# Performance work log

Hardware: AMD Instinct MI355X
Metric: run time of the kernel (lower is better)

Reference implementation:

```python
import jax, jax.numpy as jnp
import numpy as np

N = 200000      # nodes
E = 1600000     # directed edges (before self-loops)
G = 5000        # graphs (molecules)
IN, HID, OUT, HEADS = 128, 128, 128, 3


def gat_layer(x, src, dst, W, a_src, a_dst, b, heads, out_dim, concat):
    n = x.shape[0]
    h = (x @ W).reshape(n, heads, out_dim)                 # [N,H,F]
    al_s = jnp.einsum('nhf,hf->nh', h, a_src)              # [N,H]
    al_d = jnp.einsum('nhf,hf->nh', h, a_dst)
    e = jax.nn.leaky_relu(al_s[src] + al_d[dst], 0.2)      # [E,H]
    m = jax.ops.segment_max(e, dst, num_segments=n)        # softmax over incoming edges
    ex = jnp.exp(e - m[dst])
    den = jax.ops.segment_sum(ex, dst, num_segments=n)
    alpha = ex / (den[dst] + 1e-16)                        # [E,H]
    msg = h[src] * alpha[..., None]                        # [E,H,F]
    agg = jax.ops.segment_sum(msg, dst, num_segments=n)    # [N,H,F]
    agg = agg.reshape(n, heads * out_dim) if concat else agg.mean(axis=1)
    return agg + b


def setup_inputs() -> dict:
    key = jax.random.key(0)
    ks = jax.random.split(key, 16)
    d = {}
    d['x'] = jax.random.normal(ks[0], (N, IN), dtype=jnp.float32)
    d['edge_index'] = jax.random.randint(ks[1], (2, E), 0, N, dtype=jnp.int64)
    d['batch'] = jnp.sort(jax.random.randint(ks[2], (N,), 0, G, dtype=jnp.int64))
    s = 0.1
    d['W1'] = jax.random.normal(ks[3], (IN, HEADS * HID), jnp.float32) * s
    d['a1s'] = jax.random.normal(ks[4], (HEADS, HID), jnp.float32) * s
    d['a1d'] = jax.random.normal(ks[5], (HEADS, HID), jnp.float32) * s
    d['b1'] = jnp.zeros((HEADS * HID,), jnp.float32)
    d['W2'] = jax.random.normal(ks[6], (HEADS * HID, HEADS * HID), jnp.float32) * s
    d['a2s'] = jax.random.normal(ks[7], (HEADS, HID), jnp.float32) * s
    d['a2d'] = jax.random.normal(ks[8], (HEADS, HID), jnp.float32) * s
    d['b2'] = jnp.zeros((HEADS * HID,), jnp.float32)
    d['W3'] = jax.random.normal(ks[9], (HEADS * HID, OUT), jnp.float32) * s
    d['a3s'] = jax.random.normal(ks[10], (1, OUT), jnp.float32) * s
    d['a3d'] = jax.random.normal(ks[11], (1, OUT), jnp.float32) * s
    d['b3'] = jnp.zeros((OUT,), jnp.float32)
    return d


def reference(x, edge_index, batch, W1, a1s, a1d, b1, W2, a2s, a2d, b2, W3, a3s, a3d, b3):
    # PyG GATConv default add_self_loops=True
    loops = jnp.arange(N, dtype=edge_index.dtype)
    src = jnp.concatenate([edge_index[0], loops])
    dst = jnp.concatenate([edge_index[1], loops])
    h = jax.nn.leaky_relu(gat_layer(x, src, dst, W1, a1s, a1d, b1, HEADS, HID, True), 0.2)
    h = jax.nn.leaky_relu(gat_layer(h, src, dst, W2, a2s, a2d, b2, HEADS, HID, True), 0.2)
    h = jax.nn.leaky_relu(gat_layer(h, src, dst, W3, a3s, a3d, b3, 1, OUT, False), 0.2)
    # global mean pool over graphs
    sums = jax.ops.segment_sum(h, batch, num_segments=G)            # [G,OUT]
    cnt = jax.ops.segment_sum(jnp.ones((N,), h.dtype), batch, num_segments=G)
    return sums / jnp.maximum(cnt, 1.0)[:, None]
```

## Files before the change

### kernel.cpp

```cpp
#include <hip/hip_runtime.h>
#include <hip/hip_bf16.h>
#include <math.h>

#define LRELU_SLOPE 0.2f
typedef __hip_bfloat16 bf16;
typedef __hip_bfloat162 bf16x2;

typedef short s8v __attribute__((ext_vector_type(8)));
typedef float f4v __attribute__((ext_vector_type(4)));

__device__ __forceinline__ float lrelu(float v) { return v > 0.f ? v : LRELU_SLOPE * v; }
__device__ __forceinline__ float b2f(short b) {
  return __uint_as_float(((unsigned)(unsigned short)b) << 16);
}

__device__ __forceinline__ void st2(bf16* p, float x, float y) {
  float2 f{x, y};
  *(bf16x2*)p = __float22bfloat162_rn(f);
}
__device__ __forceinline__ void st2(float* p, float x, float y) {
  *(float2*)p = float2{x, y};
}

__device__ __forceinline__ void st2_nt(bf16* p, float x, float y) {
  float2 f{x, y};
  bf16x2 v = __float22bfloat162_rn(f);
  __builtin_nontemporal_store(*(unsigned int*)&v, (unsigned int*)p);
}
__device__ __forceinline__ void st2_nt(float* p, float x, float y) {
  __builtin_nontemporal_store(x, p);
  __builtin_nontemporal_store(y, p + 1);
}


__global__ void k_zero(unsigned int* __restrict__ p, long n) {
  long i = (long)blockIdx.x * blockDim.x + threadIdx.x;
  if (i < n) p[i] = 0u;
}

__global__ void k_zero_out(float* __restrict__ out, int n) {
  int i = blockIdx.x * blockDim.x + threadIdx.x;
  if (i < n) out[i] = 0.f;
}


__global__ void k_cvt(const float* __restrict__ x, bf16* __restrict__ xb, long n) {
  long i = (long)blockIdx.x * blockDim.x + threadIdx.x;
  if (i < n) xb[i] = __float2bfloat16(x[i]);
}

__global__ void k_tw(const float* __restrict__ W, bf16* __restrict__ Wt, int K, int NN) {
  int i = blockIdx.x * blockDim.x + threadIdx.x;
  if (i >= K * NN) return;
  int k = i / NN, n = i - k * NN;
  Wt[(size_t)n * K + k] = __float2bfloat16(W[i]);
}


__global__ void k_hist(const int* __restrict__ dst, int* __restrict__ deg, int E, int Et) {
  int e = blockIdx.x * blockDim.x + threadIdx.x;
  if (e >= Et) return;
  int d = (e < E) ? dst[e] : (e - E);
  atomicAdd(&deg[d], 1);
}

__global__ void k_hist1(const int* __restrict__ idx, int* __restrict__ deg, int n) {
  int i = blockIdx.x * blockDim.x + threadIdx.x;
  if (i < n) atomicAdd(&deg[idx[i]], 1);
}

__global__ void k_scan1(const int* __restrict__ deg, int* __restrict__ offs,
                        int* __restrict__ bsum, int n) {
  __shared__ int sd[256];
  int t = threadIdx.x;
  int base = blockIdx.x * 1024 + t * 4;
  int v[4]; int tsum = 0;
#pragma unroll
  for (int i = 0; i < 4; ++i) { v[i] = (base + i < n) ? deg[base + i] : 0; tsum += v[i]; }
  sd[t] = tsum;
  __syncthreads();
  for (int off = 1; off < 256; off <<= 1) {
    int x = (t >= off) ? sd[t - off] : 0;
    __syncthreads();
    sd[t] += x;
    __syncthreads();
  }
  int excl = sd[t] - tsum;
#pragma unroll
  for (int i = 0; i < 4; ++i) { if (base + i < n) offs[base + i] = excl; excl += v[i]; }
  if (t == 255) bsum[blockIdx.x] = sd[255];
}

__global__ void k_scan2(int* bsum, int nb) {
  if (threadIdx.x == 0 && blockIdx.x == 0) {
    int run = 0;
    for (int i = 0; i < nb; ++i) { int t = bsum[i]; bsum[i] = run; run += t; }
  }
}

__global__ void k_scan3(int* __restrict__ offs, const int* __restrict__ bsum, int n, int total) {
  int t = threadIdx.x;
  int base = blockIdx.x * 1024 + t * 4;
  int add = bsum[blockIdx.x];
#pragma unroll
  for (int i = 0; i < 4; ++i) if (base + i < n) offs[base + i] += add;
  if (blockIdx.x == 0 && t == 0) offs[n] = total;
}

__global__ void k_scatter(const int* __restrict__ src, const int* __restrict__ dst,
                          const int* __restrict__ offs, int* __restrict__ cur,
                          int* __restrict__ ssrc, int E, int Et) {
  int e = blockIdx.x * blockDim.x + threadIdx.x;
  if (e >= Et) return;
  int s, d;
  if (e < E) { s = src[e]; d = dst[e]; } else { s = d = e - E; }
  int pos = offs[d] + atomicAdd(&cur[d], 1);
  ssrc[pos] = s;
}


__global__ __launch_bounds__(256) void k_gemm_mfma(const bf16* __restrict__ A,
                                                   const bf16* __restrict__ Wt,
                                                   bf16* __restrict__ C,
                                                   int K, int NN) {
  __shared__ __align__(16) short sA[64 * 64];
  int t = threadIdx.x;
  int wv = t >> 6, lane = t & 63;
  int quad = lane >> 4, l15 = lane & 15;
  size_t bm0 = (size_t)blockIdx.x * 64;
  int bn0 = blockIdx.y * 64;
  const bf16* Ab = A + bm0 * K;
  const bf16* Bp = Wt + (size_t)(bn0 + wv * 16 + l15) * K;
  f4v acc[4] = {f4v{0,0,0,0}, f4v{0,0,0,0}, f4v{0,0,0,0}, f4v{0,0,0,0}};

  for (int kb = 0; kb < K; kb += 64) {
#pragma unroll
    for (int j = 0; j < 2; ++j) {
      int idx = j * 256 + t;
      int row = idx >> 3, p = idx & 7;
      int c = p ^ (row & 7);
      const bf16* g = Ab + (size_t)row * K + kb + c * 8;
      __builtin_amdgcn_global_load_lds(
          (const __attribute__((address_space(1))) void*)g,
          (__attribute__((address_space(3))) void*)((char*)sA + (size_t)(j * 256 + wv * 64) * 16),
          16, 0, 0);
    }
    __syncthreads();
#pragma unroll
    for (int kk = 0; kk < 2; ++kk) {
      s8v bfrag = *(const s8v*)(Bp + kb + kk * 32 + quad * 8);
#pragma unroll
      for (int ms = 0; ms < 4; ++ms) {
        int row = ms * 16 + l15;
        int pos = (kk * 4 + quad) ^ (row & 7);
        s8v afrag = *(const s8v*)((const char*)sA + (size_t)row * 128 + pos * 16);
        acc[ms] = __builtin_amdgcn_mfma_f32_16x16x32_bf16(afrag, bfrag, acc[ms], 0, 0, 0);
      }
    }
    __syncthreads();
  }
  int coln = bn0 + wv * 16 + l15;
#pragma unroll
  for (int ms = 0; ms < 4; ++ms)
#pragma unroll
    for (int r = 0; r < 4; ++r)
      C[(bm0 + ms * 16 + quad * 4 + r) * NN + coln] = __float2bfloat16(acc[ms][r]);
}


template <int H>
__global__ void k_al(const bf16* __restrict__ h, const float* __restrict__ as,
                     const float* __restrict__ ad, float* __restrict__ al_s,
                     float* __restrict__ al_d, int N) {
  int n = (blockIdx.x * blockDim.x + threadIdx.x) >> 6;
  int lane = threadIdx.x & 63;
  if (n >= N) return;
  int hd = lane >> 4;
  bool active = (hd < H);
  int hdc = active ? hd : 0;
  int f8 = (lane & 15) * 8;
  const bf16* hp = h + (size_t)n * (H * 128) + hdc * 128 + f8;
  s8v hv = *(const s8v*)hp;
  float ss = 0.f, sd = 0.f;
#pragma unroll
  for (int i = 0; i < 8; ++i) {
    float v = b2f(hv[i]);
    ss += v * as[hdc * 128 + f8 + i];
    sd += v * ad[hdc * 128 + f8 + i];
  }
#pragma unroll
  for (int off = 8; off; off >>= 1) {
    ss += __shfl_xor(ss, off, 64);
    sd += __shfl_xor(sd, off, 64);
  }
  if (active && (lane & 15) == 0) {
    al_s[n * H + hd] = ss;
    al_d[n * H + hd] = sd;
  }
}


template <int H, typename OT>
__global__ __launch_bounds__(256) void k_attn_agg(const bf16* __restrict__ hbuf,
                           const int* __restrict__ ssrc,
                           const int* __restrict__ offs, const float* __restrict__ al_s,
                           const float* __restrict__ al_d, const float* __restrict__ bias,
                           OT* __restrict__ out, int N) {
  constexpr int SW = (H > 1) ? 4 : 2;
  __shared__ __align__(16) float stash[4][64 * SW];
  int n = (blockIdx.x * blockDim.x + threadIdx.x) >> 6;
  int lane = threadIdx.x & 63;
  if (n >= N) return;
  float* st = stash[threadIdx.x >> 6];
  int start = offs[n], end = offs[n + 1];
  float ald[H], mx[H];
#pragma unroll
  for (int hd = 0; hd < H; ++hd) { ald[hd] = al_d[n * H + hd]; mx[hd] = -1e30f; }

  for (int pos = start + lane; pos < end; pos += 64) {
    int s = ssrc[pos];
#pragma unroll
    for (int hd = 0; hd < H; ++hd)
      mx[hd] = fmaxf(mx[hd], lrelu(al_s[s * H + hd] + ald[hd]));
  }
#pragma unroll
  for (int hd = 0; hd < H; ++hd)
#pragma unroll
    for (int off = 32; off; off >>= 1) mx[hd] = fmaxf(mx[hd], __shfl_xor(mx[hd], off, 64));

  int f0 = lane * 2;
  float den[H], accx[H], accy[H];
#pragma unroll
  for (int hd = 0; hd < H; ++hd) { den[hd] = 0.f; accx[hd] = 0.f; accy[hd] = 0.f; }

  for (int cb = start; cb < end; cb += 64) {
    int cl = end - cb; if (cl > 64) cl = 64;
    int mys = (lane < cl) ? ssrc[cb + lane] : 0;
    float myex[H];
#pragma unroll
    for (int hd = 0; hd < H; ++hd) {
      float e = lrelu(al_s[mys * H + hd] + ald[hd]);
      float ex = __expf(e - mx[hd]);
      myex[hd] = (lane < cl) ? ex : 0.f;
    }
    __builtin_amdgcn_wave_barrier();
    if (H > 1) {
      float4 s4{__int_as_float(mys), myex[0], myex[1], myex[2]};
      *(float4*)&st[lane * 4] = s4;
    } else {
      float2 s2{__int_as_float(mys), myex[0]};
      *(float2*)&st[lane * 2] = s2;
    }
    asm volatile("s_waitcnt lgkmcnt(0)" ::: "memory");
    __builtin_amdgcn_wave_barrier();

    for (int r = 0; r < cl; r += 8) {
      int su[8];
      float a[8][H];
#pragma unroll
      for (int u = 0; u < 8; ++u) {
        if (H > 1) {
          float4 ed = *(const float4*)&st[(r + u) * 4];
          su[u] = __float_as_int(ed.x);
          a[u][0] = ed.y;
          if (H > 1) { a[u][1] = ed.z; a[u][2] = ed.w; }
        } else {
          float2 ed = *(const float2*)&st[(r + u) * 2];
          su[u] = __float_as_int(ed.x);
          a[u][0] = ed.y;
        }
      }
      bf16x2 v[8][H];
#pragma unroll
      for (int u = 0; u < 8; ++u) {
        const bf16* hp = hbuf + (size_t)su[u] * (H * 128) + f0;
#pragma unroll
        for (int hd = 0; hd < H; ++hd) v[u][hd] = *(const bf16x2*)(hp + hd * 128);
      }
#pragma unroll
      for (int u = 0; u < 8; ++u)
#pragma unroll
        for (int hd = 0; hd < H; ++hd) {
          float2 f = __bfloat1622float2(v[u][hd]);
          accx[hd] += a[u][hd] * f.x;
          accy[hd] += a[u][hd] * f.y;
          if (hd == 0) {}
        }
#pragma unroll
      for (int u = 0; u < 8; ++u)
#pragma unroll
        for (int hd = 0; hd < H; ++hd) den[hd] += a[u][hd];
    }
  }
#pragma unroll
  for (int hd = 0; hd < H; ++hd) {
    float r = 1.f / (den[hd] + 1e-16f);
    float ox = lrelu(accx[hd] * r + bias[hd * 128 + f0]);
    float oy = lrelu(accy[hd] * r + bias[hd * 128 + f0 + 1]);
    st2_nt(&out[((size_t)n * H + hd) * 128 + f0], ox, oy);
  }
}


__global__ void k_pool(const float* __restrict__ h, const int* __restrict__ goffs,
                       float* __restrict__ out, int G) {
  int g = (blockIdx.x * blockDim.x + threadIdx.x) >> 6;
  int lane = threadIdx.x & 63;
  if (g >= G) return;
  int s = goffs[g], e = goffs[g + 1];
  float ax = 0.f, ay = 0.f;
  for (int n = s; n < e; ++n) {
    float2 v = *(const float2*)&h[(size_t)n * 128 + lane * 2];
    ax += v.x; ay += v.y;
  }
  float c = fmaxf((float)(e - s), 1.f);
  st2(&out[(size_t)g * 128 + lane * 2], ax / c, ay / c);
}


extern "C" void kernel_launch(void* const* d_in, const int* in_sizes, int n_in,
                              void* d_out, int out_size, void* d_ws, size_t ws_size,
                              hipStream_t stream) {
  const float* x   = (const float*)d_in[0];
  const int*   ei  = (const int*)d_in[1];
  const int*   bat = (const int*)d_in[2];
  const float* W1  = (const float*)d_in[3];
  const float* a1s = (const float*)d_in[4];
  const float* a1d = (const float*)d_in[5];
  const float* b1  = (const float*)d_in[6];
  const float* W2  = (const float*)d_in[7];
  const float* a2s = (const float*)d_in[8];
  const float* a2d = (const float*)d_in[9];
  const float* b2  = (const float*)d_in[10];
  const float* W3  = (const float*)d_in[11];
  const float* a3s = (const float*)d_in[12];
  const float* a3d = (const float*)d_in[13];
  const float* b3  = (const float*)d_in[14];
  float* out = (float*)d_out;

  const int N = in_sizes[2];
  const int E = in_sizes[1] / 2;
  const int Et = E + N;
  const int G = out_size / 128;

  char* p = (char*)d_ws;
  auto carve = [&](size_t bytes) { void* r = (void*)p; p += (bytes + 255) & ~(size_t)255; return r; };
  bf16*  bufA   = (bf16*)carve((size_t)N * 384 * 2);
  bf16*  bufB   = (bf16*)carve((size_t)N * 384 * 2);
  float* al_s   = (float*)carve((size_t)N * 3 * 4);
  float* al_d   = (float*)carve((size_t)N * 3 * 4);
  int*   ssrc   = (int*)carve((size_t)Et * 4);
  int*   offs   = (int*)carve((size_t)(N + 1) * 4);
  int*   deg    = (int*)carve((size_t)N * 4);
  int*   cur    = (int*)carve((size_t)N * 4);
  int*   bsum   = (int*)carve(4096 * 4);
  int*   gdeg   = (int*)carve((size_t)G * 4);
  int*   goffs  = (int*)carve((size_t)(G + 1) * 4);
  bf16*  Wt1    = (bf16*)carve((size_t)384 * 128 * 2);
  bf16*  Wt2    = (bf16*)carve((size_t)384 * 384 * 2);
  bf16*  Wt3    = (bf16*)carve((size_t)128 * 384 * 2);
  size_t need = (size_t)(p - (char*)d_ws);

  if (ws_size < need) {
    k_zero_out<<<(out_size + 255) / 256, 256, 0, stream>>>(out, out_size);
    return;
  }

  const int* esrc = ei;
  const int* edst = ei + E;

  int ebl = (Et + 255) / 256;
  int NB = (N + 1023) / 1024;
  int GB = (G + 1023) / 1024;
  int nodeWaveBlocks = (N * 64 + 255) / 256;

  bf16* xb = bufA;
  k_cvt<<<((long)N * 128 + 255) / 256, 256, 0, stream>>>(x, xb, (long)N * 128);
  k_tw<<<(128 * 384 + 255) / 256, 256, 0, stream>>>(W1, Wt1, 128, 384);
  k_tw<<<(384 * 384 + 255) / 256, 256, 0, stream>>>(W2, Wt2, 384, 384);
  k_tw<<<(384 * 128 + 255) / 256, 256, 0, stream>>>(W3, Wt3, 384, 128);

  k_zero<<<(N + 255) / 256, 256, 0, stream>>>((unsigned int*)deg, N);
  k_hist<<<ebl, 256, 0, stream>>>(edst, deg, E, Et);
  k_scan1<<<NB, 256, 0, stream>>>(deg, offs, bsum, N);
  k_scan2<<<1, 64, 0, stream>>>(bsum, NB);
  k_scan3<<<NB, 256, 0, stream>>>(offs, bsum, N, Et);
  k_zero<<<(N + 255) / 256, 256, 0, stream>>>((unsigned int*)cur, N);
  k_scatter<<<ebl, 256, 0, stream>>>(esrc, edst, offs, cur, ssrc, E, Et);

  k_zero<<<(G + 255) / 256, 256, 0, stream>>>((unsigned int*)gdeg, G);
  k_hist1<<<(N + 255) / 256, 256, 0, stream>>>(bat, gdeg, N);
  k_scan1<<<GB, 256, 0, stream>>>(gdeg, goffs, bsum, G);
  k_scan2<<<1, 64, 0, stream>>>(bsum, GB);
  k_scan3<<<GB, 256, 0, stream>>>(goffs, bsum, G, N);

  dim3 g1(N / 64, 6), g2(N / 64, 6), g3(N / 64, 2);

  k_gemm_mfma<<<g1, 256, 0, stream>>>(xb, Wt1, bufB, 128, 384);
  k_al<3><<<nodeWaveBlocks, 256, 0, stream>>>(bufB, a1s, a1d, al_s, al_d, N);
  k_attn_agg<3, bf16><<<nodeWaveBlocks, 256, 0, stream>>>(bufB, ssrc, offs, al_s, al_d, b1, bufA, N);

  k_gemm_mfma<<<g2, 256, 0, stream>>>(bufA, Wt2, bufB, 384, 384);
  k_al<3><<<nodeWaveBlocks, 256, 0, stream>>>(bufB, a2s, a2d, al_s, al_d, N);
  k_attn_agg<3, bf16><<<nodeWaveBlocks, 256, 0, stream>>>(bufB, ssrc, offs, al_s, al_d, b2, bufA, N);

  k_gemm_mfma<<<g3, 256, 0, stream>>>(bufA, Wt3, bufB, 384, 128);
  k_al<1><<<nodeWaveBlocks, 256, 0, stream>>>(bufB, a3s, a3d, al_s, al_d, N);
  float* out3 = (float*)bufA;
  k_attn_agg<1, float><<<nodeWaveBlocks, 256, 0, stream>>>(bufB, ssrc, offs, al_s, al_d, b3, out3, N);

  k_pool<<<(G * 64 + 255) / 256, 256, 0, stream>>>(out3, goffs, out, G);
}
```

Measured before the change: 1.469 ms.

## Fuse attention logits into GEMM epilogue, drop softmax max pass, interleave heads

The attention-coefficient dot products move into the MFMA GEMM epilogue, which reduces across lanes with shuffles and accumulates into zeroed al_s/al_d buffers with atomics. This removes the separate k_al kernels. The softmax no longer does a separate max pass; it exponentiates clamped logits directly and accumulates the denominator with wave shuffles. The GEMM output is stored head-interleaved per feature, so each lane in the aggregation reads contiguous bf16 values across all heads. In exchange there are many float atomics and extra zeroing launches, and the unshifted exp relies on logits staying small.

```diff
diff --git a/kernel.cpp b/kernel.cpp
--- a/kernel.cpp
+++ b/kernel.cpp
@@ -119,10 +119,16 @@
 }
 
 
+template <int H>
 __global__ __launch_bounds__(256) void k_gemm_mfma(const bf16* __restrict__ A,
                                                    const bf16* __restrict__ Wt,
                                                    bf16* __restrict__ C,
-                                                   int K, int NN) {
+                                                   const float* __restrict__ as,
+                                                   const float* __restrict__ ad,
+                                                   float* __restrict__ al_s,
+                                                   float* __restrict__ al_d,
+                                                   int K) {
+  constexpr int NN = H * 128;
   __shared__ __align__(16) short sA[64 * 64];
   int t = threadIdx.x;
   int wv = t >> 6, lane = t & 63;
@@ -160,43 +166,27 @@
     __syncthreads();
   }
   int coln = bn0 + wv * 16 + l15;
+  int f = coln & 127, hd = coln >> 7;
+  int cix = f * H + hd;
+  float asv = as[coln], adv = ad[coln];
 #pragma unroll
   for (int ms = 0; ms < 4; ++ms)
 #pragma unroll
-    for (int r = 0; r < 4; ++r)
-      C[(bm0 + ms * 16 + quad * 4 + r) * NN + coln] = __float2bfloat16(acc[ms][r]);
-}
-
-
-template <int H>
-__global__ void k_al(const bf16* __restrict__ h, const float* __restrict__ as,
-                     const float* __restrict__ ad, float* __restrict__ al_s,
-                     float* __restrict__ al_d, int N) {
-  int n = (blockIdx.x * blockDim.x + threadIdx.x) >> 6;
-  int lane = threadIdx.x & 63;
-  if (n >= N) return;
-  int hd = lane >> 4;
-  bool active = (hd < H);
-  int hdc = active ? hd : 0;
-  int f8 = (lane & 15) * 8;
-  const bf16* hp = h + (size_t)n * (H * 128) + hdc * 128 + f8;
-  s8v hv = *(const s8v*)hp;
-  float ss = 0.f, sd = 0.f;
-#pragma unroll
-  for (int i = 0; i < 8; ++i) {
-    float v = b2f(hv[i]);
-    ss += v * as[hdc * 128 + f8 + i];
-    sd += v * ad[hdc * 128 + f8 + i];
-  }
-#pragma unroll
-  for (int off = 8; off; off >>= 1) {
-    ss += __shfl_xor(ss, off, 64);
-    sd += __shfl_xor(sd, off, 64);
-  }
-  if (active && (lane & 15) == 0) {
-    al_s[n * H + hd] = ss;
-    al_d[n * H + hd] = sd;
-  }
+    for (int r = 0; r < 4; ++r) {
+      float v = acc[ms][r];
+      size_t row = bm0 + ms * 16 + quad * 4 + r;
+      C[row * NN + cix] = __float2bfloat16(v);
+      float vs = v * asv, vd = v * adv;
+#pragma unroll
+      for (int off = 1; off <= 8; off <<= 1) {
+        vs += __shfl_xor(vs, off, 64);
+        vd += __shfl_xor(vd, off, 64);
+      }
+      if (l15 == 0) {
+        atomicAdd(&al_s[row * H + hd], vs);
+        atomicAdd(&al_d[row * H + hd], vd);
+      }
+    }
 }
 
 
@@ -213,20 +203,9 @@
   if (n >= N) return;
   float* st = stash[threadIdx.x >> 6];
   int start = offs[n], end = offs[n + 1];
-  float ald[H], mx[H];
-#pragma unroll
-  for (int hd = 0; hd < H; ++hd) { ald[hd] = al_d[n * H + hd]; mx[hd] = -1e30f; }
-
-  for (int pos = start + lane; pos < end; pos += 64) {
-    int s = ssrc[pos];
-#pragma unroll
-    for (int hd = 0; hd < H; ++hd)
-      mx[hd] = fmaxf(mx[hd], lrelu(al_s[s * H + hd] + ald[hd]));
-  }
-#pragma unroll
-  for (int hd = 0; hd < H; ++hd)
-#pragma unroll
-    for (int off = 32; off; off >>= 1) mx[hd] = fmaxf(mx[hd], __shfl_xor(mx[hd], off, 64));
+  float ald[H];
+#pragma unroll
+  for (int hd = 0; hd < H; ++hd) ald[hd] = al_d[n * H + hd];
 
   int f0 = lane * 2;
   float den[H], accx[H], accy[H];
@@ -240,12 +219,19 @@
 #pragma unroll
     for (int hd = 0; hd < H; ++hd) {
       float e = lrelu(al_s[mys * H + hd] + ald[hd]);
-      float ex = __expf(e - mx[hd]);
+      float ex = __expf(fminf(e, 80.f));
       myex[hd] = (lane < cl) ? ex : 0.f;
+    }
+#pragma unroll
+    for (int hd = 0; hd < H; ++hd) {
+      float d = myex[hd];
+#pragma unroll
+      for (int off = 32; off; off >>= 1) d += __shfl_xor(d, off, 64);
+      den[hd] += d;
     }
     __builtin_amdgcn_wave_barrier();
     if (H > 1) {
-      float4 s4{__int_as_float(mys), myex[0], myex[1], myex[2]};
+      float4 s4{__int_as_float(mys), myex[0], myex[H > 1 ? 1 : 0], myex[H > 1 ? 2 : 0]};
       *(float4*)&st[lane * 4] = s4;
     } else {
       float2 s2{__int_as_float(mys), myex[0]};
@@ -263,33 +249,47 @@
           float4 ed = *(const float4*)&st[(r + u) * 4];
           su[u] = __float_as_int(ed.x);
           a[u][0] = ed.y;
-          if (H > 1) { a[u][1] = ed.z; a[u][2] = ed.w; }
+          a[u][H > 1 ? 1 : 0] = ed.z;
+          a[u][H > 1 ? 2 : 0] = ed.w;
         } else {
           float2 ed = *(const float2*)&st[(r + u) * 2];
           su[u] = __float_as_int(ed.x);
           a[u][0] = ed.y;
         }
       }
-      bf16x2 v[8][H];
-#pragma unroll
-      for (int u = 0; u < 8; ++u) {
-        const bf16* hp = hbuf + (size_t)su[u] * (H * 128) + f0;
-#pragma unroll
-        for (int hd = 0; hd < H; ++hd) v[u][hd] = *(const bf16x2*)(hp + hd * 128);
+      if (H > 1) {
+        bf16x2 v0[8], v1[8], v2[8];
+#pragma unroll
+        for (int u = 0; u < 8; ++u) {
+          const bf16* hp = hbuf + (size_t)su[u] * (H * 128) + f0 * H;
+          v0[u] = *(const bf16x2*)(hp);
+          v1[u] = *(const bf16x2*)(hp + 2);
+          v2[u] = *(const bf16x2*)(hp + 4);
+        }
+#pragma unroll
+        for (int u = 0; u < 8; ++u) {
+          float2 p0 = __bfloat1622float2(v0[u]);
+          float2 p1 = __bfloat1622float2(v1[u]);
+          float2 p2 = __bfloat1622float2(v2[u]);
+          accx[0] += a[u][0] * p0.x;
+          accx[H > 1 ? 1 : 0] += a[u][H > 1 ? 1 : 0] * p0.y;
+          accx[H > 1 ? 2 : 0] += a[u][H > 1 ? 2 : 0] * p1.x;
+          accy[0] += a[u][0] * p1.y;
+          accy[H > 1 ? 1 : 0] += a[u][H > 1 ? 1 : 0] * p2.x;
+          accy[H > 1 ? 2 : 0] += a[u][H > 1 ? 2 : 0] * p2.y;
+        }
+      } else {
+        bf16x2 v[8];
+#pragma unroll
+        for (int u = 0; u < 8; ++u)
+          v[u] = *(const bf16x2*)(hbuf + (size_t)su[u] * 128 + f0);
+#pragma unroll
+        for (int u = 0; u < 8; ++u) {
+          float2 fv = __bfloat1622float2(v[u]);
+          accx[0] += a[u][0] * fv.x;
+          accy[0] += a[u][0] * fv.y;
+        }
       }
-#pragma unroll
-      for (int u = 0; u < 8; ++u)
-#pragma unroll
-        for (int hd = 0; hd < H; ++hd) {
-          float2 f = __bfloat1622float2(v[u][hd]);
-          accx[hd] += a[u][hd] * f.x;
-          accy[hd] += a[u][hd] * f.y;
-          if (hd == 0) {}
-        }
-#pragma unroll
-      for (int u = 0; u < 8; ++u)
-#pragma unroll
-        for (int hd = 0; hd < H; ++hd) den[hd] += a[u][hd];
     }
   }
 #pragma unroll
@@ -373,6 +373,7 @@
   int NB = (N + 1023) / 1024;
   int GB = (G + 1023) / 1024;
   int nodeWaveBlocks = (N * 64 + 255) / 256;
+  int alZeroBlocks = (N * 6 + 255) / 256;
 
   bf16* xb = bufA;
   k_cvt<<<((long)N * 128 + 255) / 256, 256, 0, stream>>>(x, xb, (long)N * 128);
@@ -394,18 +395,18 @@
   k_scan2<<<1, 64, 0, stream>>>(bsum, GB);
   k_scan3<<<GB, 256, 0, stream>>>(goffs, bsum, G, N);
 
-  dim3 g1(N / 64, 6), g2(N / 64, 6), g3(N / 64, 2);
-
-  k_gemm_mfma<<<g1, 256, 0, stream>>>(xb, Wt1, bufB, 128, 384);
-  k_al<3><<<nodeWaveBlocks, 256, 0, stream>>>(bufB, a1s, a1d, al_s, al_d, N);
+  dim3 g6(N / 64, 6), g2(N / 64, 2);
+
+  k_zero<<<alZeroBlocks, 256, 0, stream>>>((unsigned int*)al_s, (long)N * 6);
+  k_gemm_mfma<3><<<g6, 256, 0, stream>>>(xb, Wt1, bufB, a1s, a1d, al_s, al_d, 128);
   k_attn_agg<3, bf16><<<nodeWaveBlocks, 256, 0, stream>>>(bufB, ssrc, offs, al_s, al_d, b1, bufA, N);
 
-  k_gemm_mfma<<<g2, 256, 0, stream>>>(bufA, Wt2, bufB, 384, 384);
-  k_al<3><<<nodeWaveBlocks, 256, 0, stream>>>(bufB, a2s, a2d, al_s, al_d, N);
+  k_zero<<<alZeroBlocks, 256, 0, stream>>>((unsigned int*)al_s, (long)N * 6);
+  k_gemm_mfma<3><<<g6, 256, 0, stream>>>(bufA, Wt2, bufB, a2s, a2d, al_s, al_d, 384);
   k_attn_agg<3, bf16><<<nodeWaveBlocks, 256, 0, stream>>>(bufB, ssrc, offs, al_s, al_d, b2, bufA, N);
 
-  k_gemm_mfma<<<g3, 256, 0, stream>>>(bufA, Wt3, bufB, 384, 128);
-  k_al<1><<<nodeWaveBlocks, 256, 0, stream>>>(bufB, a3s, a3d, al_s, al_d, N);
+  k_zero<<<alZeroBlocks, 256, 0, stream>>>((unsigned int*)al_s, (long)N * 6);
+  k_gemm_mfma<1><<<g2, 256, 0, stream>>>(bufA, Wt3, bufB, a3s, a3d, al_s, al_d, 384);
   float* out3 = (float*)bufA;
   k_attn_agg<1, float><<<nodeWaveBlocks, 256, 0, stream>>>(bufB, ssrc, offs, al_s, al_d, b3, out3, N);
 
```

Measured after the change: 2.139 ms. 45.6% more time.
